# Kernel tuning notes

Measured on AMD Instinct MI355X. Metric: run time of the kernel, lower is better.

Reference implementation:

```python
import jax, jax.numpy as jnp
import numpy as np

D_MODEL = 1024
NUM_HEADS = 16
HEAD_DIM = D_MODEL // NUM_HEADS
WINDOW = 256
NEG = -1000000000.0


def setup_inputs() -> dict:
    key = jax.random.key(0)
    ks = jax.random.split(key, 9)
    B, N, D = 2, 2048, D_MODEL
    s = 1.0 / np.sqrt(D)
    inp = {
        "x": jax.random.normal(ks[0], (B, N, D), dtype=jnp.float32),
        "Wq": jax.random.normal(ks[1], (D, D), dtype=jnp.float32) * s,
        "bq": jnp.zeros((D,), dtype=jnp.float32),
        "Wk": jax.random.normal(ks[2], (D, D), dtype=jnp.float32) * s,
        "bk": jnp.zeros((D,), dtype=jnp.float32),
        "Wv": jax.random.normal(ks[3], (D, D), dtype=jnp.float32) * s,
        "bv": jnp.zeros((D,), dtype=jnp.float32),
        "Wo": jax.random.normal(ks[4], (D, D), dtype=jnp.float32) * s,
        "bo": jnp.zeros((D,), dtype=jnp.float32),
    }
    return inp


def reference(x, Wq, bq, Wk, bk, Wv, bv, Wo, bo):
    B, N, D = x.shape
    H, hd = NUM_HEADS, HEAD_DIM
    q = (x @ Wq + bq).reshape(B, N, H, hd).transpose(0, 2, 1, 3)  # [B,H,N,hd]
    k = (x @ Wk + bk).reshape(B, N, H, hd).transpose(0, 2, 1, 3)
    v = (x @ Wv + bv).reshape(B, N, H, hd).transpose(0, 2, 1, 3)

    i = jnp.arange(N)[:, None]
    j = jnp.arange(N)[None, :]
    blocked = (j > i) | (j < i - WINDOW)  # causal + local window
    mask = jnp.where(blocked, jnp.float32(NEG), jnp.float32(0.0))  # [N,N]

    logits = jnp.einsum("bhid,bhjd->bhij", q, k) / jnp.sqrt(jnp.float32(hd))
    logits = logits + mask[None, None, :, :]
    attn = jax.nn.softmax(logits, axis=-1)
    out = jnp.einsum("bhij,bhjd->bhid", attn, v)  # [B,H,N,hd]
    out = out.transpose(0, 2, 1, 3).reshape(B, N, D)
    return out @ Wo + bo
```

## Files before the change

### kernel.cpp

```cpp
#include <hip/hip_runtime.h>


typedef unsigned short ushort_t;
typedef __bf16 bf16x8 __attribute__((ext_vector_type(8)));
typedef float f32x4 __attribute__((ext_vector_type(4)));
typedef unsigned short ushort8 __attribute__((ext_vector_type(8)));

#define LOG2E 1.4426950408889634f

static __device__ __forceinline__ ushort_t f2b(float f) {
    union { float f; unsigned int u; } x;
    x.f = f;
    unsigned int u = x.u;
    unsigned int r = (u + 0x7FFFu + ((u >> 16) & 1u)) >> 16;
    return (ushort_t)r;
}

static __device__ __forceinline__ void store_out(float* p, float v) { *p = v; }
static __device__ __forceinline__ void store_out(ushort_t* p, float v) { *p = f2b(v); }

static __device__ __forceinline__ void gload_lds16(const ushort_t* g, ushort_t* l) {
    __builtin_amdgcn_global_load_lds(
        (const __attribute__((address_space(1))) void*)g,
        (__attribute__((address_space(3))) void*)l, 16, 0, 0);
}

__global__ __launch_bounds__(256) void cast_f32_bf16_kernel(
    const float* __restrict__ in, ushort_t* __restrict__ out) {
    int i = (blockIdx.x * 256 + threadIdx.x) * 8;
    f32x4 a = *(const f32x4*)&in[i];
    f32x4 b = *(const f32x4*)&in[i + 4];
    ushort8 o;
#pragma unroll
    for (int e = 0; e < 4; e++) o[e] = f2b(a[e]);
#pragma unroll
    for (int e = 0; e < 4; e++) o[4 + e] = f2b(b[e]);
    *(ushort8*)&out[i] = o;
}

__global__ __launch_bounds__(256) void transpose_cast_kernel(
    const float* __restrict__ W0, const float* __restrict__ W1,
    const float* __restrict__ W2, const float* __restrict__ W3,
    ushort_t* __restrict__ T0, ushort_t* __restrict__ T1,
    ushort_t* __restrict__ T2, ushort_t* __restrict__ T3) {
    __shared__ ushort_t tile[32][33];
    const float* W;
    ushort_t* T;
    switch (blockIdx.z) {
        case 0: W = W0; T = T0; break;
        case 1: W = W1; T = T1; break;
        case 2: W = W2; T = T2; break;
        default: W = W3; T = T3; break;
    }
    int tx = threadIdx.x, ty = threadIdx.y;
    int x = blockIdx.x * 32 + tx;
    int ybase = blockIdx.y * 32 + ty;
#pragma unroll
    for (int r = 0; r < 4; r++) tile[ty + r * 8][tx] = f2b(W[(ybase + r * 8) * 1024 + x]);
    __syncthreads();
    int xo = blockIdx.y * 32 + tx;
    int yobase = blockIdx.x * 32 + ty;
#pragma unroll
    for (int r = 0; r < 4; r++) T[(yobase + r * 8) * 1024 + xo] = tile[tx][ty + r * 8];
}

template <typename OutT, int MODE, int MF>
__global__ __launch_bounds__(256) void gemm_bt_kernel(
    const ushort_t* __restrict__ A,
    const ushort_t* __restrict__ Bt0, const ushort_t* __restrict__ Bt1,
    const ushort_t* __restrict__ Bt2,
    const float* __restrict__ bias0, const float* __restrict__ bias1,
    const float* __restrict__ bias2,
    OutT* __restrict__ C0, OutT* __restrict__ C1, OutT* __restrict__ C2,
    float os0, float os1, float os2) {
    __shared__ ushort_t Al[MF * 32 * 64];
    __shared__ ushort_t Bl[128 * 64];

    const int id = blockIdx.x;
    const int xcd = id & 7;
    const int s = id >> 3;
    int m_blk, ncol, zsel;
    if (MODE == 0) {
        m_blk = (xcd >> 1) * 8 + (s & 7);
        ncol = (xcd & 1) * 12 + (s >> 3);
        zsel = ncol >> 3;
        ncol &= 7;
    } else {
        m_blk = xcd * 8 + (s & 7);
        ncol = s >> 3;
        zsel = 0;
    }
    const int m0 = m_blk * (MF * 32);
    const int n0 = ncol * 128;

    const ushort_t* Bt;
    const float* bias;
    OutT* C;
    float oscale;
    if (zsel == 0) { Bt = Bt0; bias = bias0; C = C0; oscale = os0; }
    else if (zsel == 1) { Bt = Bt1; bias = bias1; C = C1; oscale = os1; }
    else { Bt = Bt2; bias = bias2; C = C2; oscale = os2; }

    const int tid = threadIdx.x;
    const int w = tid >> 6;
    const int l = tid & 63;
    const int wm = (w >> 1) * (MF * 16);
    const int wn = (w & 1) * 64;
    const int lrow = l & 15;
    const int lq = l >> 4;

    f32x4 acc[MF][4];
#pragma unroll
    for (int mi = 0; mi < MF; mi++)
#pragma unroll
        for (int ni = 0; ni < 4; ni++) acc[mi][ni] = 0.0f;

    for (int kt = 0; kt < 1024; kt += 64) {
#pragma unroll
        for (int t = 0; t < MF; t++) {
            int idx = t * 256 + tid;
            gload_lds16(&A[(long)(m0 + (idx >> 3)) * 1024 + kt + (idx & 7) * 8], &Al[idx * 8]);
        }
#pragma unroll
        for (int t = 0; t < 4; t++) {
            int idx = t * 256 + tid;
            gload_lds16(&Bt[(long)(n0 + (idx >> 3)) * 1024 + kt + (idx & 7) * 8], &Bl[idx * 8]);
        }
        __syncthreads();
#pragma unroll
        for (int ks = 0; ks < 64; ks += 32) {
            bf16x8 af[MF], bfr[4];
#pragma unroll
            for (int mi = 0; mi < MF; mi++)
                af[mi] = *(const bf16x8*)&Al[(wm + mi * 16 + lrow) * 64 + ks + lq * 8];
#pragma unroll
            for (int ni = 0; ni < 4; ni++)
                bfr[ni] = *(const bf16x8*)&Bl[(wn + ni * 16 + lrow) * 64 + ks + lq * 8];
#pragma unroll
            for (int mi = 0; mi < MF; mi++)
#pragma unroll
                for (int ni = 0; ni < 4; ni++)
                    acc[mi][ni] = __builtin_amdgcn_mfma_f32_16x16x32_bf16(
                        af[mi], bfr[ni], acc[mi][ni], 0, 0, 0);
        }
        __syncthreads();
    }

    if (MODE == 0 && zsel == 2) {
#pragma unroll
        for (int ni = 0; ni < 4; ni++) {
            int n = n0 + wn + ni * 16 + lrow;
            int h = n >> 6, d = n & 63;
            float bv = bias[n];
#pragma unroll
            for (int mi = 0; mi < MF; mi++) {
#pragma unroll
                for (int r = 0; r < 4; r++) {
                    int m = m0 + wm + mi * 16 + lq * 4 + r;
                    long dst = ((long)(((m >> 11) << 4) + h) * 64 + d) * 2048 + (m & 2047);
                    store_out(&C[dst], acc[mi][ni][r] + bv);
                }
            }
        }
    } else {
#pragma unroll
        for (int ni = 0; ni < 4; ni++) {
            int n = n0 + wn + ni * 16 + lrow;
            float bv = bias[n];
#pragma unroll
            for (int mi = 0; mi < MF; mi++) {
#pragma unroll
                for (int r = 0; r < 4; r++) {
                    int m = m0 + wm + mi * 16 + lq * 4 + r;
                    store_out(&C[(long)m * 1024 + n], (acc[mi][ni][r] + bv) * oscale);
                }
            }
        }
    }
}

__global__ __launch_bounds__(256) void attn_kernel(
    const ushort_t* __restrict__ Q, const ushort_t* __restrict__ K,
    const ushort_t* __restrict__ VT, ushort_t* __restrict__ O) {
    __shared__ ushort_t Kl[128 * 64];
    __shared__ ushort_t Vt[64 * 136];
    __shared__ ushort_t Pb[4 * 16 * 40];

    const int id = blockIdx.x;
    const int xcd = id & 7;
    const int s = id >> 3;
    const int bh = xcd * 4 + (s >> 5);
    const int b = bh >> 4;
    const int h = bh & 15;
    const int i0 = (s & 31) * 64;

    const int tid = threadIdx.x;
    const int w = tid >> 6;
    const int l = tid & 63;
    const int lrow = l & 15;
    const int lq = l >> 4;
    const int q0 = i0 + w * 16;

    const long baseBH = ((long)b * 2048) * 1024 + (long)h * 64;
    const long baseVT = (long)bh * 64 * 2048;

    const ushort_t* qrow = Q + baseBH + (long)(q0 + lrow) * 1024;
    bf16x8 aq0 = *(const bf16x8*)&qrow[lq * 8];
    bf16x8 aq1 = *(const bf16x8*)&qrow[32 + lq * 8];

    float lpart[4];
    f32x4 oacc[4];
#pragma unroll
    for (int r = 0; r < 4; r++) lpart[r] = 0.0f;
#pragma unroll
    for (int ni = 0; ni < 4; ni++) oacc[ni] = 0.0f;

    const int kstart = (i0 - 256) > 0 ? (i0 - 256) : 0;
    const int kend = i0 + 64;
    ushort_t* Pw = &Pb[w * 16 * 40];

    for (int cs = kstart; cs < kend; cs += 128) {
#pragma unroll
        for (int t = 0; t < 4; t++) {
            int idx = t * 256 + tid;
            int key = cs + (idx >> 3);
            key = key < 2047 ? key : 2047;
            gload_lds16(&K[baseBH + (long)key * 1024 + (idx & 7) * 8], &Kl[idx * 8]);
        }
#pragma unroll
        for (int j = 0; j < 4; j++) {
            int idx = j * 256 + tid;
            int d = idx >> 4;
            int kk = (idx & 15) * 8;
            int key = cs + kk;
            key = key <= 2040 ? key : 2040;
            ushort8 vv = *(const ushort8*)&VT[baseVT + (long)d * 2048 + key];
            *(ushort8*)&Vt[d * 136 + kk] = vv;
        }
        __syncthreads();

        const int ce = (cs + 128 < kend) ? cs + 128 : kend;
        for (int kb = cs; kb < ce; kb += 32) {
            if (kb > q0 + 15 || kb + 31 < q0 - 256) continue;
            const int rb = kb - cs;
            f32x4 S0 = 0.0f, S1 = 0.0f;
            {
                bf16x8 bk;
                bk = *(const bf16x8*)&Kl[(rb + lrow) * 64 + lq * 8];
                S0 = __builtin_amdgcn_mfma_f32_16x16x32_bf16(aq0, bk, S0, 0, 0, 0);
                bk = *(const bf16x8*)&Kl[(rb + lrow) * 64 + 32 + lq * 8];
                S0 = __builtin_amdgcn_mfma_f32_16x16x32_bf16(aq1, bk, S0, 0, 0, 0);
                bk = *(const bf16x8*)&Kl[(rb + 16 + lrow) * 64 + lq * 8];
                S1 = __builtin_amdgcn_mfma_f32_16x16x32_bf16(aq0, bk, S1, 0, 0, 0);
                bk = *(const bf16x8*)&Kl[(rb + 16 + lrow) * 64 + 32 + lq * 8];
                S1 = __builtin_amdgcn_mfma_f32_16x16x32_bf16(aq1, bk, S1, 0, 0, 0);
            }
            const int col0 = kb + lrow;
            const int col1 = kb + 16 + lrow;
#pragma unroll
            for (int r = 0; r < 4; r++) {
                const int i = q0 + lq * 4 + r;
                float p0 = (col0 > i || col0 < i - 256) ? 0.0f : exp2f(S0[r] * LOG2E);
                float p1 = (col1 > i || col1 < i - 256) ? 0.0f : exp2f(S1[r] * LOG2E);
                lpart[r] += p0 + p1;
                const int prow = lq * 4 + r;
                Pw[prow * 40 + lrow] = f2b(p0);
                Pw[prow * 40 + 16 + lrow] = f2b(p1);
            }
            bf16x8 pf = *(const bf16x8*)&Pw[lrow * 40 + lq * 8];
#pragma unroll
            for (int ni = 0; ni < 4; ni++) {
                bf16x8 vf = *(const bf16x8*)&Vt[(ni * 16 + lrow) * 136 + rb + lq * 8];
                oacc[ni] = __builtin_amdgcn_mfma_f32_16x16x32_bf16(pf, vf, oacc[ni], 0, 0, 0);
            }
        }
        __syncthreads();
    }

    float lS[4];
#pragma unroll
    for (int r = 0; r < 4; r++) {
        float rs = lpart[r];
#pragma unroll
        for (int off = 8; off; off >>= 1) rs += __shfl_xor(rs, off, 64);
        lS[r] = rs;
    }

#pragma unroll
    for (int ni = 0; ni < 4; ni++) {
#pragma unroll
        for (int r = 0; r < 4; r++) {
            const int i = q0 + lq * 4 + r;
            const int d = ni * 16 + lrow;
            O[baseBH + (long)i * 1024 + d] = f2b(oacc[ni][r] / lS[r]);
        }
    }
}

extern "C" void kernel_launch(void* const* d_in, const int* in_sizes, int n_in,
                              void* d_out, int out_size, void* d_ws, size_t ws_size,
                              hipStream_t stream) {
    const float* x  = (const float*)d_in[0];
    const float* Wq = (const float*)d_in[1];
    const float* bq = (const float*)d_in[2];
    const float* Wk = (const float*)d_in[3];
    const float* bk = (const float*)d_in[4];
    const float* Wv = (const float*)d_in[5];
    const float* bv = (const float*)d_in[6];
    const float* Wo = (const float*)d_in[7];
    const float* bo = (const float*)d_in[8];
    float* out = (float*)d_out;

    ushort_t* ws = (ushort_t*)d_ws;
    const size_t WMAT = (size_t)1024 * 1024;
    const size_t ACT = (size_t)2 * 2048 * 1024;
    ushort_t* xbf = ws;
    ushort_t* Wqt = xbf + ACT;
    ushort_t* Wkt = Wqt + WMAT;
    ushort_t* Wvt = Wkt + WMAT;
    ushort_t* Wot = Wvt + WMAT;
    ushort_t* qws = Wot + WMAT;
    ushort_t* kws = qws + ACT;
    ushort_t* vtws = kws + ACT;
    ushort_t* aws = xbf;

    cast_f32_bf16_kernel<<<dim3((unsigned)(ACT / 2048)), 256, 0, stream>>>(x, xbf);

    transpose_cast_kernel<<<dim3(32, 32, 4), dim3(32, 8), 0, stream>>>(
        Wq, Wk, Wv, Wo, Wqt, Wkt, Wvt, Wot);

    gemm_bt_kernel<ushort_t, 0, 4><<<768, 256, 0, stream>>>(
        xbf, Wqt, Wkt, Wvt, bq, bk, bv, qws, kws, vtws, 0.125f, 1.0f, 1.0f);

    attn_kernel<<<1024, 256, 0, stream>>>(qws, kws, vtws, aws);

    gemm_bt_kernel<float, 1, 2><<<512, 256, 0, stream>>>(
        aws, Wot, Wot, Wot, bo, bo, bo, out, out, out, 1.0f, 1.0f, 1.0f);
}
```

Before: 198.2 us.

## Shrink GEMM M-tiles, vectorize V^T stores, and read K/V directly in attention

Both projection GEMMs now use half the M-tile per block and launch twice as many blocks, to raise occupancy and parallelism. The transposed-V epilogue packs four bf16 values into one vector store instead of four scalar stores. The attention kernel drops its shared-memory staging of K and V and the block-wide barriers. Each wave now loads K and V fragments straight from global memory for only its own window of 32-key blocks. This removes sync and LDS traffic, but blocks no longer share K/V loads, which increases global/L2 reads.

```diff
diff --git a/kernel.cpp b/kernel.cpp
--- a/kernel.cpp
+++ b/kernel.cpp
@@ -5,6 +5,7 @@
 typedef __bf16 bf16x8 __attribute__((ext_vector_type(8)));
 typedef float f32x4 __attribute__((ext_vector_type(4)));
 typedef unsigned short ushort8 __attribute__((ext_vector_type(8)));
+typedef unsigned short ushort4_t __attribute__((ext_vector_type(4)));
 
 #define LOG2E 1.4426950408889634f
 
@@ -64,7 +65,7 @@
     for (int r = 0; r < 4; r++) T[(yobase + r * 8) * 1024 + xo] = tile[tx][ty + r * 8];
 }
 
-template <typename OutT, int MODE, int MF>
+template <typename OutT, int MODE>
 __global__ __launch_bounds__(256) void gemm_bt_kernel(
     const ushort_t* __restrict__ A,
     const ushort_t* __restrict__ Bt0, const ushort_t* __restrict__ Bt1,
@@ -73,6 +74,7 @@
     const float* __restrict__ bias2,
     OutT* __restrict__ C0, OutT* __restrict__ C1, OutT* __restrict__ C2,
     float os0, float os1, float os2) {
+    constexpr int MF = (MODE == 0) ? 2 : 1;
     __shared__ ushort_t Al[MF * 32 * 64];
     __shared__ ushort_t Bl[128 * 64];
 
@@ -81,13 +83,13 @@
     const int s = id >> 3;
     int m_blk, ncol, zsel;
     if (MODE == 0) {
-        m_blk = (xcd >> 1) * 8 + (s & 7);
-        ncol = (xcd & 1) * 12 + (s >> 3);
+        m_blk = (xcd >> 1) * 16 + (s & 15);
+        ncol = (xcd & 1) * 12 + (s >> 4);
         zsel = ncol >> 3;
         ncol &= 7;
     } else {
-        m_blk = xcd * 8 + (s & 7);
-        ncol = s >> 3;
+        m_blk = xcd * 16 + (s & 15);
+        ncol = s >> 4;
         zsel = 0;
     }
     const int m0 = m_blk * (MF * 32);
@@ -146,34 +148,37 @@
         __syncthreads();
     }
 
-    if (MODE == 0 && zsel == 2) {
-#pragma unroll
-        for (int ni = 0; ni < 4; ni++) {
-            int n = n0 + wn + ni * 16 + lrow;
-            int h = n >> 6, d = n & 63;
-            float bv = bias[n];
-#pragma unroll
-            for (int mi = 0; mi < MF; mi++) {
-#pragma unroll
-                for (int r = 0; r < 4; r++) {
-                    int m = m0 + wm + mi * 16 + lq * 4 + r;
+    if constexpr (MODE == 0) {
+        if (zsel == 2) {
+            ushort_t* Cv = (ushort_t*)C;
+#pragma unroll
+            for (int ni = 0; ni < 4; ni++) {
+                int n = n0 + wn + ni * 16 + lrow;
+                int h = n >> 6, d = n & 63;
+                float bv = bias[n];
+#pragma unroll
+                for (int mi = 0; mi < MF; mi++) {
+                    int m = m0 + wm + mi * 16 + lq * 4;
+                    ushort4_t u;
+#pragma unroll
+                    for (int r = 0; r < 4; r++) u[r] = f2b(acc[mi][ni][r] + bv);
                     long dst = ((long)(((m >> 11) << 4) + h) * 64 + d) * 2048 + (m & 2047);
-                    store_out(&C[dst], acc[mi][ni][r] + bv);
+                    *(ushort4_t*)&Cv[dst] = u;
                 }
             }
-        }
-    } else {
-#pragma unroll
-        for (int ni = 0; ni < 4; ni++) {
-            int n = n0 + wn + ni * 16 + lrow;
-            float bv = bias[n];
-#pragma unroll
-            for (int mi = 0; mi < MF; mi++) {
-#pragma unroll
-                for (int r = 0; r < 4; r++) {
-                    int m = m0 + wm + mi * 16 + lq * 4 + r;
-                    store_out(&C[(long)m * 1024 + n], (acc[mi][ni][r] + bv) * oscale);
-                }
+            return;
+        }
+    }
+#pragma unroll
+    for (int ni = 0; ni < 4; ni++) {
+        int n = n0 + wn + ni * 16 + lrow;
+        float bv = bias[n];
+#pragma unroll
+        for (int mi = 0; mi < MF; mi++) {
+#pragma unroll
+            for (int r = 0; r < 4; r++) {
+                int m = m0 + wm + mi * 16 + lq * 4 + r;
+                store_out(&C[(long)m * 1024 + n], (acc[mi][ni][r] + bv) * oscale);
             }
         }
     }
@@ -182,8 +187,6 @@
 __global__ __launch_bounds__(256) void attn_kernel(
     const ushort_t* __restrict__ Q, const ushort_t* __restrict__ K,
     const ushort_t* __restrict__ VT, ushort_t* __restrict__ O) {
-    __shared__ ushort_t Kl[128 * 64];
-    __shared__ ushort_t Vt[64 * 136];
     __shared__ ushort_t Pb[4 * 16 * 40];
 
     const int id = blockIdx.x;
@@ -202,7 +205,8 @@
     const int q0 = i0 + w * 16;
 
     const long baseBH = ((long)b * 2048) * 1024 + (long)h * 64;
-    const long baseVT = (long)bh * 64 * 2048;
+    const ushort_t* Kb = K + baseBH;
+    const ushort_t* Vb = VT + (long)bh * 64 * 2048;
 
     const ushort_t* qrow = Q + baseBH + (long)(q0 + lrow) * 1024;
     bf16x8 aq0 = *(const bf16x8*)&qrow[lq * 8];
@@ -215,66 +219,42 @@
 #pragma unroll
     for (int ni = 0; ni < 4; ni++) oacc[ni] = 0.0f;
 
-    const int kstart = (i0 - 256) > 0 ? (i0 - 256) : 0;
-    const int kend = i0 + 64;
     ushort_t* Pw = &Pb[w * 16 * 40];
-
-    for (int cs = kstart; cs < kend; cs += 128) {
-#pragma unroll
-        for (int t = 0; t < 4; t++) {
-            int idx = t * 256 + tid;
-            int key = cs + (idx >> 3);
-            key = key < 2047 ? key : 2047;
-            gload_lds16(&K[baseBH + (long)key * 1024 + (idx & 7) * 8], &Kl[idx * 8]);
-        }
-#pragma unroll
-        for (int j = 0; j < 4; j++) {
-            int idx = j * 256 + tid;
-            int d = idx >> 4;
-            int kk = (idx & 15) * 8;
-            int key = cs + kk;
-            key = key <= 2040 ? key : 2040;
-            ushort8 vv = *(const ushort8*)&VT[baseVT + (long)d * 2048 + key];
-            *(ushort8*)&Vt[d * 136 + kk] = vv;
-        }
-        __syncthreads();
-
-        const int ce = (cs + 128 < kend) ? cs + 128 : kend;
-        for (int kb = cs; kb < ce; kb += 32) {
-            if (kb > q0 + 15 || kb + 31 < q0 - 256) continue;
-            const int rb = kb - cs;
-            f32x4 S0 = 0.0f, S1 = 0.0f;
-            {
-                bf16x8 bk;
-                bk = *(const bf16x8*)&Kl[(rb + lrow) * 64 + lq * 8];
-                S0 = __builtin_amdgcn_mfma_f32_16x16x32_bf16(aq0, bk, S0, 0, 0, 0);
-                bk = *(const bf16x8*)&Kl[(rb + lrow) * 64 + 32 + lq * 8];
-                S0 = __builtin_amdgcn_mfma_f32_16x16x32_bf16(aq1, bk, S0, 0, 0, 0);
-                bk = *(const bf16x8*)&Kl[(rb + 16 + lrow) * 64 + lq * 8];
-                S1 = __builtin_amdgcn_mfma_f32_16x16x32_bf16(aq0, bk, S1, 0, 0, 0);
-                bk = *(const bf16x8*)&Kl[(rb + 16 + lrow) * 64 + 32 + lq * 8];
-                S1 = __builtin_amdgcn_mfma_f32_16x16x32_bf16(aq1, bk, S1, 0, 0, 0);
-            }
-            const int col0 = kb + lrow;
-            const int col1 = kb + 16 + lrow;
-#pragma unroll
-            for (int r = 0; r < 4; r++) {
-                const int i = q0 + lq * 4 + r;
-                float p0 = (col0 > i || col0 < i - 256) ? 0.0f : exp2f(S0[r] * LOG2E);
-                float p1 = (col1 > i || col1 < i - 256) ? 0.0f : exp2f(S1[r] * LOG2E);
-                lpart[r] += p0 + p1;
-                const int prow = lq * 4 + r;
-                Pw[prow * 40 + lrow] = f2b(p0);
-                Pw[prow * 40 + 16 + lrow] = f2b(p1);
-            }
-            bf16x8 pf = *(const bf16x8*)&Pw[lrow * 40 + lq * 8];
-#pragma unroll
-            for (int ni = 0; ni < 4; ni++) {
-                bf16x8 vf = *(const bf16x8*)&Vt[(ni * 16 + lrow) * 136 + rb + lq * 8];
-                oacc[ni] = __builtin_amdgcn_mfma_f32_16x16x32_bf16(pf, vf, oacc[ni], 0, 0, 0);
-            }
-        }
-        __syncthreads();
+    const int kb_lo = (q0 >= 256) ? ((q0 - 256) & ~31) : 0;
+    const int kb_hi = (q0 + 15) & ~31;
+
+    for (int kb = kb_lo; kb <= kb_hi; kb += 32) {
+        bf16x8 vf[4];
+#pragma unroll
+        for (int ni = 0; ni < 4; ni++)
+            vf[ni] = *(const bf16x8*)&Vb[(long)(ni * 16 + lrow) * 2048 + kb + lq * 8];
+        bf16x8 bk00 = *(const bf16x8*)&Kb[(long)(kb + lrow) * 1024 + lq * 8];
+        bf16x8 bk01 = *(const bf16x8*)&Kb[(long)(kb + lrow) * 1024 + 32 + lq * 8];
+        bf16x8 bk10 = *(const bf16x8*)&Kb[(long)(kb + 16 + lrow) * 1024 + lq * 8];
+        bf16x8 bk11 = *(const bf16x8*)&Kb[(long)(kb + 16 + lrow) * 1024 + 32 + lq * 8];
+
+        f32x4 S0 = 0.0f, S1 = 0.0f;
+        S0 = __builtin_amdgcn_mfma_f32_16x16x32_bf16(aq0, bk00, S0, 0, 0, 0);
+        S0 = __builtin_amdgcn_mfma_f32_16x16x32_bf16(aq1, bk01, S0, 0, 0, 0);
+        S1 = __builtin_amdgcn_mfma_f32_16x16x32_bf16(aq0, bk10, S1, 0, 0, 0);
+        S1 = __builtin_amdgcn_mfma_f32_16x16x32_bf16(aq1, bk11, S1, 0, 0, 0);
+
+        const int col0 = kb + lrow;
+        const int col1 = kb + 16 + lrow;
+#pragma unroll
+        for (int r = 0; r < 4; r++) {
+            const int i = q0 + lq * 4 + r;
+            float p0 = (col0 > i || col0 < i - 256) ? 0.0f : exp2f(S0[r] * LOG2E);
+            float p1 = (col1 > i || col1 < i - 256) ? 0.0f : exp2f(S1[r] * LOG2E);
+            lpart[r] += p0 + p1;
+            const int prow = lq * 4 + r;
+            Pw[prow * 40 + lrow] = f2b(p0);
+            Pw[prow * 40 + 16 + lrow] = f2b(p1);
+        }
+        bf16x8 pf = *(const bf16x8*)&Pw[lrow * 40 + lq * 8];
+#pragma unroll
+        for (int ni = 0; ni < 4; ni++)
+            oacc[ni] = __builtin_amdgcn_mfma_f32_16x16x32_bf16(pf, vf[ni], oacc[ni], 0, 0, 0);
     }
 
     float lS[4];
@@ -329,11 +309,11 @@
     transpose_cast_kernel<<<dim3(32, 32, 4), dim3(32, 8), 0, stream>>>(
         Wq, Wk, Wv, Wo, Wqt, Wkt, Wvt, Wot);
 
-    gemm_bt_kernel<ushort_t, 0, 4><<<768, 256, 0, stream>>>(
+    gemm_bt_kernel<ushort_t, 0><<<1536, 256, 0, stream>>>(
         xbf, Wqt, Wkt, Wvt, bq, bk, bv, qws, kws, vtws, 0.125f, 1.0f, 1.0f);
 
     attn_kernel<<<1024, 256, 0, stream>>>(qws, kws, vtws, aws);
 
-    gemm_bt_kernel<float, 1, 2><<<512, 256, 0, stream>>>(
+    gemm_bt_kernel<float, 1><<<1024, 256, 0, stream>>>(
         aws, Wot, Wot, Wot, bo, bo, bo, out, out, out, 1.0f, 1.0f, 1.0f);
 }
```

After: 200.7 us. Within noise of the previous version (+1.2%).
